# Performance work log

Hardware: AMD Instinct MI355X
Metric: run time of the kernel (lower is better)

## Reference

```python
import jax, jax.numpy as jnp
import numpy as np

N = 50000        # num graph nodes
E = 800000       # num edges (before self-loops)
IN_DIM = 128     # input feature dim
HID = 32         # hidden dim per head
HEADS1 = 4       # gat1 heads (concat)
AGENTS = 32      # num_agents
NEG_SLOPE = 0.2  # PyG GATConv default leaky_relu slope


def setup_inputs() -> dict:
    key = jax.random.key(0)
    ks = jax.random.split(key, 16)
    s = 0.1
    x = jax.random.normal(ks[0], (N, IN_DIM), jnp.float32)
    edge_index = jax.random.randint(ks[1], (2, E), 0, N, dtype=jnp.int64)
    # GATConv layer 1: in=128 -> heads=4, out=32 (concat -> 128)
    W1 = jax.random.normal(ks[2], (IN_DIM, HEADS1 * HID), jnp.float32) * s
    a1s = jax.random.normal(ks[3], (HEADS1, HID), jnp.float32) * s
    a1d = jax.random.normal(ks[4], (HEADS1, HID), jnp.float32) * s
    b1 = jnp.zeros((HEADS1 * HID,), jnp.float32)
    # GATConv layer 2: in=128 -> heads=1, out=32
    W2 = jax.random.normal(ks[5], (HEADS1 * HID, 1 * HID), jnp.float32) * s
    a2s = jax.random.normal(ks[6], (1, HID), jnp.float32) * s
    a2d = jax.random.normal(ks[7], (1, HID), jnp.float32) * s
    b2 = jnp.zeros((HID,), jnp.float32)
    # actor / critic heads
    Wa = jax.random.normal(ks[8], (HID, AGENTS), jnp.float32) * s
    ba = jnp.zeros((AGENTS,), jnp.float32)
    Wc = jax.random.normal(ks[9], (HID, 1), jnp.float32) * s
    bc = jnp.zeros((1,), jnp.float32)
    return {"x": x, "edge_index": edge_index,
            "W1": W1, "a1s": a1s, "a1d": a1d, "b1": b1,
            "W2": W2, "a2s": a2s, "a2d": a2d, "b2": b2,
            "Wa": Wa, "ba": ba, "Wc": Wc, "bc": bc}


def gat_layer(x, edge_index, W, a_src, a_dst, b, heads, out_ch):
    """PyG-style GATConv: self-loops, per-edge attention, segment softmax over
    incoming edges of each target node, scatter-add aggregation, concat heads."""
    n = x.shape[0]
    loop = jnp.arange(n, dtype=edge_index.dtype)
    src = jnp.concatenate([edge_index[0], loop])  # message source j
    dst = jnp.concatenate([edge_index[1], loop])  # message target i
    h = (x @ W).reshape(n, heads, out_ch)                     # [N,H,F]
    a_s = jnp.sum(h * a_src, axis=-1)                         # [N,H]
    a_d = jnp.sum(h * a_dst, axis=-1)                         # [N,H]
    e = jax.nn.leaky_relu(a_s[src] + a_d[dst], NEG_SLOPE)     # [E',H]
    m = jax.ops.segment_max(e, dst, num_segments=n)           # per-target max
    ex = jnp.exp(e - m[dst])
    den = jax.ops.segment_sum(ex, dst, num_segments=n)
    alpha = ex / den[dst]                                     # [E',H]
    out = jax.ops.segment_sum(alpha[:, :, None] * h[src], dst, num_segments=n)
    return out.reshape(n, heads * out_ch) + b


def reference(x, edge_index, W1, a1s, a1d, b1, W2, a2s, a2d, b2, Wa, ba, Wc, bc):
    h = jax.nn.elu(gat_layer(x, edge_index, W1, a1s, a1d, b1, HEADS1, HID))
    h = jax.nn.elu(gat_layer(h, edge_index, W2, a2s, a2d, b2, 1, HID))
    logits = (h @ Wa + ba).T            # [AGENTS, N]
    value = (h @ Wc + bc).mean(axis=0)  # [1]
    return logits, value
```

## Files before the change

### kernel.cpp

```cpp
#include <hip/hip_runtime.h>
#include <math.h>


#define TILE 4096

typedef __attribute__((ext_vector_type(8))) short short8;
typedef __attribute__((ext_vector_type(4))) float floatx4;

__device__ __forceinline__ float leaky02(float e){ return e > 0.f ? e : 0.2f*e; }

__device__ __forceinline__ unsigned short f2bf(float f){
    union { float f; unsigned int i; } v; v.f = f;
    unsigned int r = v.i + 0x7fffu + ((v.i >> 16) & 1u);
    return (unsigned short)(r >> 16);
}
__device__ __forceinline__ float bfx(unsigned int g){
    union { unsigned int i; float f; } v; v.i = g << 16; return v.f;
}
__device__ __forceinline__ float bfy(unsigned int g){
    union { unsigned int i; float f; } v; v.i = g & 0xffff0000u; return v.f;
}
__device__ __forceinline__ float bf1(unsigned short u){
    union { unsigned int i; float f; } v; v.i = ((unsigned int)u) << 16; return v.f;
}

__global__ __launch_bounds__(256) void k_fused1(const float* __restrict__ x,
        const float* __restrict__ W1,
        const float* __restrict__ aS, const float* __restrict__ aD,
        unsigned short* __restrict__ h1b, float* __restrict__ pAS, float* __restrict__ pAD, int n,
        const int* __restrict__ ei, int e, int e2, int* __restrict__ counts, int nbT, int nbG,
        int* __restrict__ done, float* __restrict__ valbuf)
{
    __shared__ unsigned short As[64*136];
    __shared__ unsigned short Bs[128*136];
    const int tid = threadIdx.x;

    if (blockIdx.x >= nbG){
        int tb = blockIdx.x - nbG;
        int* h = (int*)As;
        h[tid] = 0; __syncthreads();
        int base = tb*TILE;
        #pragma unroll
        for (int k = 0; k < TILE/256; k++){
            int i = base + k*256 + tid;
            if (i < e2){
                int d = (i < e) ? ei[(size_t)e + i] : (i - e);
                atomicAdd(&h[d >> 8], 1);
            }
        }
        __syncthreads();
        counts[(size_t)tid*nbT + tb] = h[tid];
        return;
    }

    if (blockIdx.x == 0){
        if (tid == 0){ *done = 0; }
        for (int i = tid; i < 64*32; i += 256) valbuf[i] = 0.f;
    }

    const int brow = blockIdx.x*64;
    {
        int row = tid >> 2, cb = (tid & 3)*32;
        bool ok = brow + row < n;
        #pragma unroll
        for (int i=0;i<8;i++){
            float4 v = ok ? *(const float4*)&x[(size_t)(brow+row)*128 + cb + i*4]
                          : make_float4(0.f,0.f,0.f,0.f);
            ushort4 b = make_ushort4(f2bf(v.x),f2bf(v.y),f2bf(v.z),f2bf(v.w));
            *(ushort4*)&As[row*136 + cb + i*4] = b;
        }
    }
    {
        #pragma unroll
        for (int j=0;j<16;j++){
            int idx = tid + j*256;
            int k = idx >> 5, nn0 = (idx & 31)*4;
            float4 v = *(const float4*)&W1[(size_t)k*128 + nn0];
            Bs[(nn0+0)*136 + k] = f2bf(v.x);
            Bs[(nn0+1)*136 + k] = f2bf(v.y);
            Bs[(nn0+2)*136 + k] = f2bf(v.z);
            Bs[(nn0+3)*136 + k] = f2bf(v.w);
        }
    }
    __syncthreads();

    const int wv = tid >> 6, lane = tid & 63;
    const int m = lane & 15, quad = lane >> 4;
    floatx4 acc[8];
    #pragma unroll
    for (int i=0;i<8;i++) acc[i] = (floatx4){0.f,0.f,0.f,0.f};

    #pragma unroll
    for (int kc=0; kc<4; kc++){
        int k0 = kc*32 + quad*8;
        short8 a = *(const short8*)&As[(wv*16+m)*136 + k0];
        #pragma unroll
        for (int ct=0; ct<8; ct++){
            short8 b = *(const short8*)&Bs[(ct*16+m)*136 + k0];
            acc[ct] = __builtin_amdgcn_mfma_f32_16x16x32_bf16(a, b, acc[ct], 0,0,0);
        }
    }
    __syncthreads();

    #pragma unroll
    for (int ct=0; ct<8; ct++){
        #pragma unroll
        for (int r=0;r<4;r++){
            int row = wv*16 + quad*4 + r;
            As[row*128 + ct*16 + m] = f2bf(acc[ct][r]);
        }
    }
    __syncthreads();

    {
        int row = tid >> 2, hd = tid & 3;
        int grow = brow + row;
        if (grow < n){
            float ps=0.f, pd=0.f;
            #pragma unroll
            for (int i=0;i<4;i++){
                uint4 u = *(const uint4*)&As[row*128 + hd*32 + i*8];
                *(uint4*)&h1b[(size_t)grow*128 + hd*32 + i*8] = u;
                unsigned int uw[4] = {u.x,u.y,u.z,u.w};
                #pragma unroll
                for (int j=0;j<4;j++){
                    float c0 = bfx(uw[j]), c1 = bfy(uw[j]);
                    int cc = hd*32 + i*8 + j*2;
                    ps += c0*aS[cc] + c1*aS[cc+1];
                    pd += c0*aD[cc] + c1*aD[cc+1];
                }
            }
            pAS[grow*4+hd] = ps;
            pAD[grow*4+hd] = pd;
        }
    }
}

__global__ __launch_bounds__(256) void k_scan(int* __restrict__ counts, int nb,
        int* __restrict__ digTot, int* __restrict__ base257, int* __restrict__ done)
{
    __shared__ int sb[256];
    __shared__ int lastF;
    const int t = blockIdx.x;
    const int i = threadIdx.x;
    int carry = 0;
    for (int c0 = 0; c0 < nb; c0 += 256){
        int idx = c0 + i;
        int v = (idx < nb) ? counts[(size_t)t*nb + idx] : 0;
        sb[i] = v; __syncthreads();
        for (int off = 1; off < 256; off <<= 1){
            int u = (i >= off) ? sb[i-off] : 0;
            __syncthreads();
            if (i >= off) sb[i] += u;
            __syncthreads();
        }
        if (idx < nb) counts[(size_t)t*nb + idx] = carry + sb[i] - v;
        int tot = sb[255];
        __syncthreads();
        carry += tot;
    }
    if (i == 0){
        atomicExch(&digTot[t], carry);
        __threadfence();
        int tk = atomicAdd(done, 1);
        lastF = (tk == 255);
    }
    __syncthreads();
    if (lastF){
        __threadfence();
        int v = atomicAdd(&digTot[i], 0);
        sb[i] = v; __syncthreads();
        for (int off = 1; off < 256; off <<= 1){
            int u = (i >= off) ? sb[i-off] : 0;
            __syncthreads();
            if (i >= off) sb[i] += u;
            __syncthreads();
        }
        base257[i] = sb[i] - v;
        if (i == 255) base257[256] = sb[255];
    }
}

__global__ __launch_bounds__(256) void k_bucket(const int* __restrict__ ei, int e, int e2,
        const int* __restrict__ counts, int nbT, const int* __restrict__ base257,
        unsigned int* __restrict__ buck)
{
    __shared__ int curs[256];
    int t = threadIdx.x;
    curs[t] = counts[(size_t)t*nbT + blockIdx.x] + base257[t];
    __syncthreads();
    int base = blockIdx.x*TILE;
    #pragma unroll
    for (int k = 0; k < TILE/256; k++){
        int i = base + k*256 + t;
        if (i < e2){
            int s, d;
            if (i < e){ s = ei[i]; d = ei[(size_t)e + i]; }
            else      { s = i - e; d = i - e; }
            int p = atomicAdd(&curs[d >> 8], 1);
            buck[p] = ((unsigned int)d << 16) | (unsigned int)s;
        }
    }
}

__global__ __launch_bounds__(256) void k_p2(const unsigned int* __restrict__ buck,
        const int* __restrict__ base257, int n,
        int* __restrict__ csr, int* __restrict__ rs, int* __restrict__ re)
{
    __shared__ int bins[256], sc[256], curs[256];
    const int b = blockIdx.x, t = threadIdx.x;
    const int lo = base257[b], hi = base257[b+1];
    bins[t] = 0; __syncthreads();
    for (int i = lo + t; i < hi; i += 256){
        int dg = (buck[i] >> 16) & 0xFF;
        atomicAdd(&bins[dg], 1);
    }
    __syncthreads();
    sc[t] = bins[t]; __syncthreads();
    for (int off = 1; off < 256; off <<= 1){
        int v = (t >= off) ? sc[t-off] : 0;
        __syncthreads();
        if (t >= off) sc[t] += v;
        __syncthreads();
    }
    int sInc = sc[t];
    int node = b*256 + t;
    if (node < n){
        rs[node] = lo + sInc - bins[t];
        re[node] = lo + sInc;
    }
    curs[t] = lo + sInc - bins[t];
    __syncthreads();
    for (int i = lo + t; i < hi; i += 256){
        unsigned int pk = buck[i];
        int p = atomicAdd(&curs[(pk >> 16) & 0xFF], 1);
        csr[p] = (int)(pk & 0xFFFFu);
    }
}

__global__ __launch_bounds__(256) void k_agg1(const int* __restrict__ rs, const int* __restrict__ re,
        const int* __restrict__ csr, const float* __restrict__ as1, const float* __restrict__ ad1,
        const unsigned short* __restrict__ h1b, const float* __restrict__ b1,
        unsigned short* __restrict__ h1ob, int n)
{
    const int lane = threadIdx.x & 63;
    const int node = blockIdx.x*4 + (threadIdx.x >> 6);
    if (node >= n) return;
    const int h   = lane >> 4;
    const int f   = lane*2;
    const int j16 = lane & 15;
    const int grp = lane & 48;
    const float adv = ad1[node*4 + h];
    const int start = rs[node], end = re[node];
    const unsigned int* hp = (const unsigned int*)h1b + (f >> 1);

    float den = 0.f, ax = 0.f, ay = 0.f;
    int i0 = start;

    for (; i0 + 16 <= end; i0 += 16){
        int sj = csr[i0 + j16];
        float e = __expf(leaky02(as1[sj*4 + h] + adv));
        den += e;
        #pragma unroll
        for (int j = 0; j < 16; j++){
            float ej = __shfl(e,  grp + j, 64);
            int   s2 = __shfl(sj, grp + j, 64);
            unsigned int g = hp[s2*64];
            ax += ej*bfx(g); ay += ej*bfy(g);
        }
    }
    int c = end - i0;
    if (c > 0){
        int jj = (j16 < c) ? j16 : (c-1);
        int sj = csr[i0 + jj];
        float e = __expf(leaky02(as1[sj*4 + h] + adv));
        if (j16 < c) den += e;
        for (int j = 0; j < c; j += 4){
            #pragma unroll
            for (int u = 0; u < 4; u++){
                int je = j + u;
                int jc = (je < c) ? je : (c-1);
                float ej = __shfl(e,  grp + jc, 64);
                int   s2 = __shfl(sj, grp + jc, 64);
                ej = (je < c) ? ej : 0.f;
                unsigned int g = hp[s2*64];
                ax += ej*bfx(g); ay += ej*bfy(g);
            }
        }
    }
    den += __shfl_xor(den, 1, 64);
    den += __shfl_xor(den, 2, 64);
    den += __shfl_xor(den, 4, 64);
    den += __shfl_xor(den, 8, 64);

    float ox = ax/den + b1[f];
    float oy = ay/den + b1[f+1];
    ox = ox > 0.f ? ox : expm1f(ox);
    oy = oy > 0.f ? oy : expm1f(oy);
    unsigned int pk = (unsigned int)f2bf(ox) | ((unsigned int)f2bf(oy) << 16);
    *(unsigned int*)&h1ob[(size_t)node*128 + f] = pk;
}

__global__ __launch_bounds__(256) void k_gemm2(const unsigned short* __restrict__ h1ob,
        const float* __restrict__ W2,
        const float* __restrict__ aS, const float* __restrict__ aD,
        unsigned short* __restrict__ h2pb, float* __restrict__ pAS, float* __restrict__ pAD, int n)
{
    __shared__ unsigned short As[64*136];
    __shared__ unsigned short Bs[32*136];
    const int tid  = threadIdx.x;
    const int brow = blockIdx.x*64;

    {
        int row = tid >> 2, cb = (tid & 3)*32;
        bool ok = brow + row < n;
        #pragma unroll
        for (int i=0;i<4;i++){
            uint4 v = ok ? *(const uint4*)&h1ob[(size_t)(brow+row)*128 + cb + i*8]
                         : make_uint4(0,0,0,0);
            *(uint4*)&As[row*136 + cb + i*8] = v;
        }
    }
    {
        #pragma unroll
        for (int j=0;j<4;j++){
            int idx = tid + j*256;
            int k = idx >> 3, nn0 = (idx & 7)*4;
            float4 v = *(const float4*)&W2[(size_t)k*32 + nn0];
            Bs[(nn0+0)*136 + k] = f2bf(v.x);
            Bs[(nn0+1)*136 + k] = f2bf(v.y);
            Bs[(nn0+2)*136 + k] = f2bf(v.z);
            Bs[(nn0+3)*136 + k] = f2bf(v.w);
        }
    }
    __syncthreads();

    const int wv = tid >> 6, lane = tid & 63;
    const int m = lane & 15, quad = lane >> 4;
    floatx4 acc[2];
    acc[0] = (floatx4){0.f,0.f,0.f,0.f};
    acc[1] = (floatx4){0.f,0.f,0.f,0.f};

    #pragma unroll
    for (int kc=0; kc<4; kc++){
        int k0 = kc*32 + quad*8;
        short8 a = *(const short8*)&As[(wv*16+m)*136 + k0];
        #pragma unroll
        for (int ct=0; ct<2; ct++){
            short8 b = *(const short8*)&Bs[(ct*16+m)*136 + k0];
            acc[ct] = __builtin_amdgcn_mfma_f32_16x16x32_bf16(a, b, acc[ct], 0,0,0);
        }
    }
    __syncthreads();

    #pragma unroll
    for (int ct=0; ct<2; ct++){
        #pragma unroll
        for (int r=0;r<4;r++){
            int row = wv*16 + quad*4 + r;
            As[row*32 + ct*16 + m] = f2bf(acc[ct][r]);
        }
    }
    __syncthreads();

    if (tid < 64){
        int grow = brow + tid;
        if (grow < n){
            float ps=0.f, pd=0.f;
            #pragma unroll
            for (int i=0;i<4;i++){
                uint4 u = *(const uint4*)&As[tid*32 + i*8];
                *(uint4*)&h2pb[(size_t)grow*32 + i*8] = u;
                unsigned int uw[4] = {u.x,u.y,u.z,u.w};
                #pragma unroll
                for (int j=0;j<4;j++){
                    float c0 = bfx(uw[j]), c1 = bfy(uw[j]);
                    int cc = i*8 + j*2;
                    ps += c0*aS[cc] + c1*aS[cc+1];
                    pd += c0*aD[cc] + c1*aD[cc+1];
                }
            }
            pAS[grow] = ps;
            pAD[grow] = pd;
        }
    }
}

__global__ __launch_bounds__(256) void k_agg2h(const int* __restrict__ rs, const int* __restrict__ re,
        const int* __restrict__ csr, const float* __restrict__ as2, const float* __restrict__ ad2,
        const unsigned short* __restrict__ h2pb, const float* __restrict__ b2,
        const float* __restrict__ Wa, const float* __restrict__ ba, const float* __restrict__ Wc,
        int n, float* __restrict__ out, float* __restrict__ valbuf)
{
    __shared__ float WaS[1024], WcS[32], baS[32], b2S[32];
    __shared__ float h2s[4*32], vpart[4], logit_s[128];
    const int tid = threadIdx.x;

    *(float4*)&WaS[tid*4] = *(const float4*)&Wa[tid*4];
    if (tid < 32){ WcS[tid] = Wc[tid]; baS[tid] = ba[tid]; b2S[tid] = b2[tid]; }
    __syncthreads();

    const int lane = tid & 63, wv = tid >> 6;
    const int node = blockIdx.x*4 + wv;
    const int f    = lane & 31;
    const int half = lane >> 5;
    const int j16  = lane & 15;
    const int grp  = lane & 48;
    const bool valid = node < n;

    float den = 0.f, acc = 0.f;
    if (valid){
        const float adv = ad2[node];
        const int start = rs[node], end = re[node];
        const unsigned short* hp = h2pb + f;
        int i0 = start;
        for (; i0 + 16 <= end; i0 += 16){
            int sj = csr[i0 + j16];
            float e = __expf(leaky02(as2[sj] + adv));
            den += e;
            #pragma unroll
            for (int jj = 0; jj < 8; jj++){
                int j = 2*jj + half;
                float ej = __shfl(e,  grp + j, 64);
                int   s2 = __shfl(sj, grp + j, 64);
                acc += ej * bf1(hp[s2*32]);
            }
        }
        int c = end - i0;
        if (c > 0){
            int jj = (j16 < c) ? j16 : (c-1);
            int sj = csr[i0 + jj];
            float e = __expf(leaky02(as2[sj] + adv));
            if (j16 < c) den += e;
            for (int j = half; j < c; j += 8){
                #pragma unroll
                for (int u = 0; u < 4; u++){
                    int je = j + 2*u;
                    int jc = (je < c) ? je : (c-1);
                    float ej = __shfl(e,  grp + (jc & 15), 64);
                    int   s2 = __shfl(sj, grp + (jc & 15), 64);
                    ej = (je < c) ? ej : 0.f;
                    acc += ej * bf1(hp[s2*32]);
                }
            }
        }
    }
    den += __shfl_xor(den, 1, 64);
    den += __shfl_xor(den, 2, 64);
    den += __shfl_xor(den, 4, 64);
    den += __shfl_xor(den, 8, 64);
    acc += __shfl_xor(acc, 32, 64);

    if (valid && half == 0){
        float o = acc/den + b2S[f];
        o = o > 0.f ? o : expm1f(o);
        h2s[wv*32 + f] = o;
    }

    {
        float t = 0.f;
        if (valid && half == 0) t = h2s[wv*32 + f] * WcS[f];
        t += __shfl_xor(t, 1, 64);
        t += __shfl_xor(t, 2, 64);
        t += __shfl_xor(t, 4, 64);
        t += __shfl_xor(t, 8, 64);
        t += __shfl_xor(t, 16, 64);
        if (lane == 0) vpart[wv] = valid ? t : 0.f;
    }

    {
        float pa = 0.f;
        if (valid){
            int a = lane & 31;
            #pragma unroll
            for (int cc = 0; cc < 16; cc++){
                int c = half*16 + cc;
                pa += h2s[wv*32 + c] * WaS[c*32 + a];
            }
        }
        pa += __shfl_xor(pa, 32, 64);
        if (valid && half == 0) logit_s[wv*32 + (lane & 31)] = pa + baS[lane & 31];
    }
    __syncthreads();

    if (tid < 128){
        int a = tid >> 2, nd = tid & 3;
        int nodeS = blockIdx.x*4 + nd;
        if (nodeS < n) out[(size_t)a*n + nodeS] = logit_s[nd*32 + a];
    }
    if (tid == 0){
        float bp = vpart[0] + vpart[1] + vpart[2] + vpart[3];
        atomicAdd(&valbuf[(blockIdx.x & 63)*32], bp);
    }
}

__global__ void k_val(float* __restrict__ valbuf, const float* __restrict__ bc,
                      int n, float* __restrict__ out)
{
    int tid = threadIdx.x;
    float v = atomicAdd(&valbuf[tid*32], 0.f);
    v += __shfl_xor(v, 1, 64);
    v += __shfl_xor(v, 2, 64);
    v += __shfl_xor(v, 4, 64);
    v += __shfl_xor(v, 8, 64);
    v += __shfl_xor(v, 16, 64);
    v += __shfl_xor(v, 32, 64);
    if (tid == 0) out[(size_t)32*n] = v*(1.0f/n) + bc[0];
}

extern "C" void kernel_launch(void* const* d_in, const int* in_sizes, int n_in,
                              void* d_out, int out_size, void* d_ws, size_t ws_size,
                              hipStream_t stream)
{
    const float* x   = (const float*)d_in[0];
    const int*   ei  = (const int*)d_in[1];
    const float* W1  = (const float*)d_in[2];
    const float* a1s = (const float*)d_in[3];
    const float* a1d = (const float*)d_in[4];
    const float* b1  = (const float*)d_in[5];
    const float* W2  = (const float*)d_in[6];
    const float* a2s = (const float*)d_in[7];
    const float* a2d = (const float*)d_in[8];
    const float* b2  = (const float*)d_in[9];
    const float* Wa  = (const float*)d_in[10];
    const float* ba  = (const float*)d_in[11];
    const float* Wc  = (const float*)d_in[12];
    const float* bc  = (const float*)d_in[13];
    float* out = (float*)d_out;

    const int N  = in_sizes[0] / 128;
    const int E  = in_sizes[1] / 2;
    const int E2 = E + N;
    const int nbT = (E2 + TILE - 1) / TILE;
    const int nbB = (N + 255) / 256;
    const int nbG = (N + 63) / 64;
    const int nbAgg = (N + 3) / 4;

    char* base = (char*)d_ws;
    auto alloc = [&](size_t bytes) -> char* {
        char* p = base; base += (bytes + 255) & ~(size_t)255; return p;
    };
    float* as1    = (float*)alloc((size_t)N*4*4);
    float* ad1    = (float*)alloc((size_t)N*4*4);
    float* as2    = (float*)alloc((size_t)N*4);
    float* ad2    = (float*)alloc((size_t)N*4);
    int* counts   = (int*)alloc((size_t)nbT*256*4);
    int* digTot   = (int*)alloc(256*4);
    int* base257  = (int*)alloc(257*4);
    int* done     = (int*)alloc(256);
    float* valbuf = (float*)alloc(64*32*4);
    int* rs       = (int*)alloc((size_t)N*4);
    int* re       = (int*)alloc((size_t)N*4);
    int* csr      = (int*)alloc((size_t)E2*4);
    unsigned int* buck = (unsigned int*)alloc((size_t)E2*4);
    unsigned short* h1b  = (unsigned short*)alloc((size_t)N*128*2);
    unsigned short* h1ob = (unsigned short*)alloc((size_t)N*128*2);
    unsigned short* h2pb = (unsigned short*)alloc((size_t)N*32*2);

    k_fused1<<<nbG + nbT, 256, 0, stream>>>(x, W1, a1s, a1d, h1b, as1, ad1, N,
                                            ei, E, E2, counts, nbT, nbG, done, valbuf);
    k_scan<<<256, 256, 0, stream>>>(counts, nbT, digTot, base257, done);
    k_bucket<<<nbT, 256, 0, stream>>>(ei, E, E2, counts, nbT, base257, buck);
    k_p2<<<nbB, 256, 0, stream>>>(buck, base257, N, csr, rs, re);
    k_agg1<<<nbAgg, 256, 0, stream>>>(rs, re, csr, as1, ad1, h1b, b1, h1ob, N);
    k_gemm2<<<nbG, 256, 0, stream>>>(h1ob, W2, a2s, a2d, h2pb, as2, ad2, N);
    k_agg2h<<<nbAgg, 256, 0, stream>>>(rs, re, csr, as2, ad2, h2pb, b2,
                                       Wa, ba, Wc, N, out, valbuf);
    k_val<<<1, 64, 0, stream>>>(valbuf, bc, N, out);
}
```

Measured before the change: 238.8 us.

## Fuse CSR build into one persistent kernel and fuse layer-1 aggregation with GEMM2

Merges the scan, bucket and per-bucket sort kernels into one 256-block kernel that uses atomic-counter grid barriers between phases, which removes two launches. Layer-1 aggregation now writes its bf16 rows straight into shared memory and feeds the layer-2 MFMA GEMM in the same block, so the h1ob intermediate no longer round-trips through global memory. The grid barriers assume all 256 blocks are resident at once, and each aggregation block now processes 64 nodes in sequence, which lowers the parallelism available to hide gather latency.

Result: slower. 283.6 us (+18.7%).

```diff
diff --git a/kernel.cpp b/kernel.cpp
--- a/kernel.cpp
+++ b/kernel.cpp
@@ -29,7 +29,7 @@
         const float* __restrict__ aS, const float* __restrict__ aD,
         unsigned short* __restrict__ h1b, float* __restrict__ pAS, float* __restrict__ pAD, int n,
         const int* __restrict__ ei, int e, int e2, int* __restrict__ counts, int nbT, int nbG,
-        int* __restrict__ done, float* __restrict__ valbuf)
+        int* __restrict__ done, int* __restrict__ done2, float* __restrict__ valbuf)
 {
     __shared__ unsigned short As[64*136];
     __shared__ unsigned short Bs[128*136];
@@ -54,7 +54,7 @@
     }
 
     if (blockIdx.x == 0){
-        if (tid == 0){ *done = 0; }
+        if (tid == 0){ *done = 0; *done2 = 0; }
         for (int i = tid; i < 64*32; i += 256) valbuf[i] = 0.f;
     }
 
@@ -136,17 +136,21 @@
     }
 }
 
-__global__ __launch_bounds__(256) void k_scan(int* __restrict__ counts, int nb,
-        int* __restrict__ digTot, int* __restrict__ base257, int* __restrict__ done)
+__global__ __launch_bounds__(256) void k_sort2(const int* __restrict__ ei, int e, int e2,
+        int* __restrict__ counts, int nbT, int* __restrict__ digTot, int* __restrict__ base257,
+        int* __restrict__ done, int* __restrict__ done2, unsigned int* __restrict__ buck,
+        int* __restrict__ csr, int* __restrict__ rs, int* __restrict__ re, int n, int nbB)
 {
     __shared__ int sb[256];
+    __shared__ int sh2[256];
     __shared__ int lastF;
     const int t = blockIdx.x;
     const int i = threadIdx.x;
+
     int carry = 0;
-    for (int c0 = 0; c0 < nb; c0 += 256){
+    for (int c0 = 0; c0 < nbT; c0 += 256){
         int idx = c0 + i;
-        int v = (idx < nb) ? counts[(size_t)t*nb + idx] : 0;
+        int v = (idx < nbT) ? counts[(size_t)t*nbT + idx] : 0;
         sb[i] = v; __syncthreads();
         for (int off = 1; off < 256; off <<= 1){
             int u = (i >= off) ? sb[i-off] : 0;
@@ -154,7 +158,7 @@
             if (i >= off) sb[i] += u;
             __syncthreads();
         }
-        if (idx < nb) counts[(size_t)t*nb + idx] = carry + sb[i] - v;
+        if (idx < nbT) counts[(size_t)t*nbT + idx] = carry + sb[i] - v;
         int tot = sb[255];
         __syncthreads();
         carry += tot;
@@ -167,7 +171,6 @@
     }
     __syncthreads();
     if (lastF){
-        __threadfence();
         int v = atomicAdd(&digTot[i], 0);
         sb[i] = v; __syncthreads();
         for (int off = 1; off < 256; off <<= 1){
@@ -178,164 +181,154 @@
         }
         base257[i] = sb[i] - v;
         if (i == 255) base257[256] = sb[255];
-    }
-}
-
-__global__ __launch_bounds__(256) void k_bucket(const int* __restrict__ ei, int e, int e2,
-        const int* __restrict__ counts, int nbT, const int* __restrict__ base257,
-        unsigned int* __restrict__ buck)
-{
-    __shared__ int curs[256];
-    int t = threadIdx.x;
-    curs[t] = counts[(size_t)t*nbT + blockIdx.x] + base257[t];
-    __syncthreads();
-    int base = blockIdx.x*TILE;
-    #pragma unroll
-    for (int k = 0; k < TILE/256; k++){
-        int i = base + k*256 + t;
-        if (i < e2){
-            int s, d;
-            if (i < e){ s = ei[i]; d = ei[(size_t)e + i]; }
-            else      { s = i - e; d = i - e; }
-            int p = atomicAdd(&curs[d >> 8], 1);
-            buck[p] = ((unsigned int)d << 16) | (unsigned int)s;
-        }
-    }
-}
-
-__global__ __launch_bounds__(256) void k_p2(const unsigned int* __restrict__ buck,
-        const int* __restrict__ base257, int n,
-        int* __restrict__ csr, int* __restrict__ rs, int* __restrict__ re)
-{
-    __shared__ int bins[256], sc[256], curs[256];
-    const int b = blockIdx.x, t = threadIdx.x;
-    const int lo = base257[b], hi = base257[b+1];
-    bins[t] = 0; __syncthreads();
-    for (int i = lo + t; i < hi; i += 256){
-        int dg = (buck[i] >> 16) & 0xFF;
-        atomicAdd(&bins[dg], 1);
-    }
-    __syncthreads();
-    sc[t] = bins[t]; __syncthreads();
-    for (int off = 1; off < 256; off <<= 1){
-        int v = (t >= off) ? sc[t-off] : 0;
-        __syncthreads();
-        if (t >= off) sc[t] += v;
-        __syncthreads();
-    }
-    int sInc = sc[t];
-    int node = b*256 + t;
-    if (node < n){
-        rs[node] = lo + sInc - bins[t];
-        re[node] = lo + sInc;
-    }
-    curs[t] = lo + sInc - bins[t];
-    __syncthreads();
-    for (int i = lo + t; i < hi; i += 256){
-        unsigned int pk = buck[i];
-        int p = atomicAdd(&curs[(pk >> 16) & 0xFF], 1);
-        csr[p] = (int)(pk & 0xFFFFu);
-    }
-}
-
-__global__ __launch_bounds__(256) void k_agg1(const int* __restrict__ rs, const int* __restrict__ re,
+        __syncthreads();
+        if (i == 0){ __threadfence(); atomicAdd(done, 1); }
+    }
+    if (i == 0){
+        while (atomicAdd(done, 0) < 257) ;
+        __threadfence();
+    }
+    __syncthreads();
+
+    if (t < nbT){
+        sh2[i] = counts[(size_t)i*nbT + t] + base257[i];
+        __syncthreads();
+        int base = t*TILE;
+        #pragma unroll
+        for (int k = 0; k < TILE/256; k++){
+            int idx = base + k*256 + i;
+            if (idx < e2){
+                int s, d;
+                if (idx < e){ s = ei[idx]; d = ei[(size_t)e + idx]; }
+                else        { s = idx - e; d = idx - e; }
+                int p = atomicAdd(&sh2[d >> 8], 1);
+                buck[p] = ((unsigned int)d << 16) | (unsigned int)s;
+            }
+        }
+    }
+    __syncthreads();
+    if (i == 0){
+        __threadfence();
+        atomicAdd(done2, 1);
+        while (atomicAdd(done2, 0) < 256) ;
+        __threadfence();
+    }
+    __syncthreads();
+
+    if (t < nbB){
+        const int lo = base257[t], hi = base257[t+1];
+        sh2[i] = 0; __syncthreads();
+        for (int idx = lo + i; idx < hi; idx += 256)
+            atomicAdd(&sh2[(buck[idx] >> 16) & 0xFF], 1);
+        __syncthreads();
+        int bv = sh2[i];
+        sb[i] = bv; __syncthreads();
+        for (int off = 1; off < 256; off <<= 1){
+            int u = (i >= off) ? sb[i-off] : 0;
+            __syncthreads();
+            if (i >= off) sb[i] += u;
+            __syncthreads();
+        }
+        int sInc = sb[i];
+        int node = t*256 + i;
+        if (node < n){
+            rs[node] = lo + sInc - bv;
+            re[node] = lo + sInc;
+        }
+        __syncthreads();
+        sh2[i] = lo + sInc - bv;
+        __syncthreads();
+        for (int idx = lo + i; idx < hi; idx += 256){
+            unsigned int pk = buck[idx];
+            int p = atomicAdd(&sh2[(pk >> 16) & 0xFF], 1);
+            csr[p] = (int)(pk & 0xFFFFu);
+        }
+    }
+}
+
+__global__ __launch_bounds__(256) void k_agg1g(const int* __restrict__ rs, const int* __restrict__ re,
         const int* __restrict__ csr, const float* __restrict__ as1, const float* __restrict__ ad1,
         const unsigned short* __restrict__ h1b, const float* __restrict__ b1,
-        unsigned short* __restrict__ h1ob, int n)
-{
-    const int lane = threadIdx.x & 63;
-    const int node = blockIdx.x*4 + (threadIdx.x >> 6);
-    if (node >= n) return;
-    const int h   = lane >> 4;
-    const int f   = lane*2;
-    const int j16 = lane & 15;
-    const int grp = lane & 48;
-    const float adv = ad1[node*4 + h];
-    const int start = rs[node], end = re[node];
-    const unsigned int* hp = (const unsigned int*)h1b + (f >> 1);
-
-    float den = 0.f, ax = 0.f, ay = 0.f;
-    int i0 = start;
-
-    for (; i0 + 16 <= end; i0 += 16){
-        int sj = csr[i0 + j16];
-        float e = __expf(leaky02(as1[sj*4 + h] + adv));
-        den += e;
-        #pragma unroll
-        for (int j = 0; j < 16; j++){
-            float ej = __shfl(e,  grp + j, 64);
-            int   s2 = __shfl(sj, grp + j, 64);
-            unsigned int g = hp[s2*64];
-            ax += ej*bfx(g); ay += ej*bfy(g);
-        }
-    }
-    int c = end - i0;
-    if (c > 0){
-        int jj = (j16 < c) ? j16 : (c-1);
-        int sj = csr[i0 + jj];
-        float e = __expf(leaky02(as1[sj*4 + h] + adv));
-        if (j16 < c) den += e;
-        for (int j = 0; j < c; j += 4){
-            #pragma unroll
-            for (int u = 0; u < 4; u++){
-                int je = j + u;
-                int jc = (je < c) ? je : (c-1);
-                float ej = __shfl(e,  grp + jc, 64);
-                int   s2 = __shfl(sj, grp + jc, 64);
-                ej = (je < c) ? ej : 0.f;
-                unsigned int g = hp[s2*64];
-                ax += ej*bfx(g); ay += ej*bfy(g);
-            }
-        }
-    }
-    den += __shfl_xor(den, 1, 64);
-    den += __shfl_xor(den, 2, 64);
-    den += __shfl_xor(den, 4, 64);
-    den += __shfl_xor(den, 8, 64);
-
-    float ox = ax/den + b1[f];
-    float oy = ay/den + b1[f+1];
-    ox = ox > 0.f ? ox : expm1f(ox);
-    oy = oy > 0.f ? oy : expm1f(oy);
-    unsigned int pk = (unsigned int)f2bf(ox) | ((unsigned int)f2bf(oy) << 16);
-    *(unsigned int*)&h1ob[(size_t)node*128 + f] = pk;
-}
-
-__global__ __launch_bounds__(256) void k_gemm2(const unsigned short* __restrict__ h1ob,
-        const float* __restrict__ W2,
-        const float* __restrict__ aS, const float* __restrict__ aD,
-        unsigned short* __restrict__ h2pb, float* __restrict__ pAS, float* __restrict__ pAD, int n)
+        const float* __restrict__ W2, const float* __restrict__ aS2, const float* __restrict__ aD2,
+        unsigned short* __restrict__ h2pb, float* __restrict__ pAS2, float* __restrict__ pAD2, int n)
 {
     __shared__ unsigned short As[64*136];
     __shared__ unsigned short Bs[32*136];
     const int tid  = threadIdx.x;
     const int brow = blockIdx.x*64;
-
-    {
-        int row = tid >> 2, cb = (tid & 3)*32;
-        bool ok = brow + row < n;
-        #pragma unroll
-        for (int i=0;i<4;i++){
-            uint4 v = ok ? *(const uint4*)&h1ob[(size_t)(brow+row)*128 + cb + i*8]
-                         : make_uint4(0,0,0,0);
-            *(uint4*)&As[row*136 + cb + i*8] = v;
-        }
-    }
-    {
-        #pragma unroll
-        for (int j=0;j<4;j++){
-            int idx = tid + j*256;
-            int k = idx >> 3, nn0 = (idx & 7)*4;
-            float4 v = *(const float4*)&W2[(size_t)k*32 + nn0];
-            Bs[(nn0+0)*136 + k] = f2bf(v.x);
-            Bs[(nn0+1)*136 + k] = f2bf(v.y);
-            Bs[(nn0+2)*136 + k] = f2bf(v.z);
-            Bs[(nn0+3)*136 + k] = f2bf(v.w);
-        }
-    }
-    __syncthreads();
-
-    const int wv = tid >> 6, lane = tid & 63;
+    const int lane = tid & 63, wv = tid >> 6;
+
+    #pragma unroll
+    for (int j=0;j<4;j++){
+        int idx = tid + j*256;
+        int k = idx >> 3, nn0 = (idx & 7)*4;
+        float4 v = *(const float4*)&W2[(size_t)k*32 + nn0];
+        Bs[(nn0+0)*136 + k] = f2bf(v.x);
+        Bs[(nn0+1)*136 + k] = f2bf(v.y);
+        Bs[(nn0+2)*136 + k] = f2bf(v.z);
+        Bs[(nn0+3)*136 + k] = f2bf(v.w);
+    }
+
+    const int h   = lane >> 4;
+    const int f   = lane*2;
+    const int j16 = lane & 15;
+    const int grp = lane & 48;
+    const unsigned int* hp = (const unsigned int*)h1b + (f >> 1);
+
+    for (int it = 0; it < 16; it++){
+        const int row  = it*4 + wv;
+        const int node = brow + row;
+        unsigned int pk = 0;
+        if (node < n){
+            const float adv = ad1[node*4 + h];
+            const int start = rs[node], end = re[node];
+            float den = 0.f, ax = 0.f, ay = 0.f;
+            int i0 = start;
+            for (; i0 + 16 <= end; i0 += 16){
+                int sj = csr[i0 + j16];
+                float e = __expf(leaky02(as1[sj*4 + h] + adv));
+                den += e;
+                #pragma unroll
+                for (int j = 0; j < 16; j++){
+                    float ej = __shfl(e,  grp + j, 64);
+                    int   s2 = __shfl(sj, grp + j, 64);
+                    unsigned int g = hp[s2*64];
+                    ax += ej*bfx(g); ay += ej*bfy(g);
+                }
+            }
+            int c = end - i0;
+            if (c > 0){
+                int jj = (j16 < c) ? j16 : (c-1);
+                int sj = csr[i0 + jj];
+                float e = __expf(leaky02(as1[sj*4 + h] + adv));
+                if (j16 < c) den += e;
+                for (int j = 0; j < c; j += 4){
+                    #pragma unroll
+                    for (int u = 0; u < 4; u++){
+                        int je = j + u;
+                        int jc = (je < c) ? je : (c-1);
+                        float ej = __shfl(e,  grp + jc, 64);
+                        int   s2 = __shfl(sj, grp + jc, 64);
+                        ej = (je < c) ? ej : 0.f;
+                        unsigned int g = hp[s2*64];
+                        ax += ej*bfx(g); ay += ej*bfy(g);
+                    }
+                }
+            }
+            den += __shfl_xor(den, 1, 64);
+            den += __shfl_xor(den, 2, 64);
+            den += __shfl_xor(den, 4, 64);
+            den += __shfl_xor(den, 8, 64);
+            float ox = ax/den + b1[f];
+            float oy = ay/den + b1[f+1];
+            ox = ox > 0.f ? ox : expm1f(ox);
+            oy = oy > 0.f ? oy : expm1f(oy);
+            pk = (unsigned int)f2bf(ox) | ((unsigned int)f2bf(oy) << 16);
+        }
+        *(unsigned int*)&As[row*136 + f] = pk;
+    }
+    __syncthreads();
+
     const int m = lane & 15, quad = lane >> 4;
     floatx4 acc[2];
     acc[0] = (floatx4){0.f,0.f,0.f,0.f};
@@ -376,12 +369,12 @@
                 for (int j=0;j<4;j++){
                     float c0 = bfx(uw[j]), c1 = bfy(uw[j]);
                     int cc = i*8 + j*2;
-                    ps += c0*aS[cc] + c1*aS[cc+1];
-                    pd += c0*aD[cc] + c1*aD[cc+1];
+                    ps += c0*aS2[cc] + c1*aS2[cc+1];
+                    pd += c0*aD2[cc] + c1*aD2[cc+1];
                 }
             }
-            pAS[grow] = ps;
-            pAD[grow] = pd;
+            pAS2[grow] = ps;
+            pAD2[grow] = pd;
         }
     }
 }
@@ -548,22 +541,21 @@
     int* digTot   = (int*)alloc(256*4);
     int* base257  = (int*)alloc(257*4);
     int* done     = (int*)alloc(256);
+    int* done2    = (int*)alloc(256);
     float* valbuf = (float*)alloc(64*32*4);
     int* rs       = (int*)alloc((size_t)N*4);
     int* re       = (int*)alloc((size_t)N*4);
     int* csr      = (int*)alloc((size_t)E2*4);
     unsigned int* buck = (unsigned int*)alloc((size_t)E2*4);
     unsigned short* h1b  = (unsigned short*)alloc((size_t)N*128*2);
-    unsigned short* h1ob = (unsigned short*)alloc((size_t)N*128*2);
     unsigned short* h2pb = (unsigned short*)alloc((size_t)N*32*2);
 
     k_fused1<<<nbG + nbT, 256, 0, stream>>>(x, W1, a1s, a1d, h1b, as1, ad1, N,
-                                            ei, E, E2, counts, nbT, nbG, done, valbuf);
-    k_scan<<<256, 256, 0, stream>>>(counts, nbT, digTot, base257, done);
-    k_bucket<<<nbT, 256, 0, stream>>>(ei, E, E2, counts, nbT, base257, buck);
-    k_p2<<<nbB, 256, 0, stream>>>(buck, base257, N, csr, rs, re);
-    k_agg1<<<nbAgg, 256, 0, stream>>>(rs, re, csr, as1, ad1, h1b, b1, h1ob, N);
-    k_gemm2<<<nbG, 256, 0, stream>>>(h1ob, W2, a2s, a2d, h2pb, as2, ad2, N);
+                                            ei, E, E2, counts, nbT, nbG, done, done2, valbuf);
+    k_sort2<<<256, 256, 0, stream>>>(ei, E, E2, counts, nbT, digTot, base257,
+                                     done, done2, buck, csr, rs, re, N, nbB);
+    k_agg1g<<<nbG, 256, 0, stream>>>(rs, re, csr, as1, ad1, h1b, b1,
+                                     W2, a2s, a2d, h2pb, as2, ad2, N);
     k_agg2h<<<nbAgg, 256, 0, stream>>>(rs, re, csr, as2, ad2, h2pb, b2,
                                        Wa, ba, Wc, N, out, valbuf);
     k_val<<<1, 64, 0, stream>>>(valbuf, bc, N, out);
```
